# Kernel tuning notes

Hardware: AMD Instinct MI355X
Metric: run time of the kernel (lower is better)

Reference implementation:

```python
import jax, jax.numpy as jnp
import numpy as np

DECAY = 0.99
EPS = 1e-5
COMMIT_W = 1.0


def setup_inputs() -> dict:
    key = jax.random.key(0)
    k1, k2, k3 = jax.random.split(key, 3)
    N, D, K = 65536, 64, 2048
    x = jax.random.normal(k1, (N, D), dtype=jnp.float32)
    embed = jax.random.normal(k2, (K, D), dtype=jnp.float32)
    embed_avg = jax.random.normal(k3, (K, D), dtype=jnp.float32)
    cluster_size = jnp.ones((K,), dtype=jnp.float32)
    return {"x": x, "embed": embed, "embed_avg": embed_avg, "cluster_size": cluster_size}


def reference(x, embed, embed_avg, cluster_size):
    # x: [N, D], embed: [K, D]
    K = embed.shape[0]
    # squared euclidean distances [N, K] (the cdist step)
    x2 = jnp.sum(x * x, axis=-1, keepdims=True)            # [N, 1]
    e2 = jnp.sum(embed * embed, axis=-1)                    # [K]
    dist = x2 - 2.0 * (x @ embed.T) + e2[None, :]           # [N, K]
    embed_ind = jnp.argmin(dist, axis=-1)                   # [N]

    # codebook gather + straight-through estimator
    quantize = embed[embed_ind]                              # [N, D]
    commit_loss = COMMIT_W * jnp.mean((jax.lax.stop_gradient(quantize) - x) ** 2)
    quantize_st = x + jax.lax.stop_gradient(quantize - x)

    # EMA codebook update (scatter / segment-sum, no gradient)
    ones = jnp.ones(embed_ind.shape, dtype=x.dtype)
    counts = jax.ops.segment_sum(ones, embed_ind, num_segments=K)        # [K]
    embed_sum = jax.ops.segment_sum(x, embed_ind, num_segments=K)        # [K, D]
    new_cluster_size = DECAY * cluster_size + (1.0 - DECAY) * counts
    new_embed_avg = DECAY * embed_avg + (1.0 - DECAY) * embed_sum
    n = jnp.sum(new_cluster_size)
    smoothed = (new_cluster_size + EPS) / (n + K * EPS) * n              # laplace smoothing
    new_embed = new_embed_avg / smoothed[:, None]                         # [K, D]

    return quantize_st, commit_loss, embed_ind, new_embed
```

## Files before the change

### kernel.cpp

```cpp
#include <hip/hip_runtime.h>
#include <hip/hip_bf16.h>

#define N_ROWS 65536
#define DIM 64
#define KC 2048
#define NPHH 16
#define DECAY_F 0.99f
#define OMD_F 0.01f
#define EPS_F 1e-5f
#define MARGIN 0.005f

typedef short  s16x8  __attribute__((ext_vector_type(8)));
typedef __bf16 bf16x8 __attribute__((ext_vector_type(8)));
typedef float  f32x4v __attribute__((ext_vector_type(4)));

__device__ __forceinline__ bf16x8 as_bf(s16x8 v) { return __builtin_bit_cast(bf16x8, v); }

static constexpr size_t WS_E2       = 0;
static constexpr size_t WS_SMOOTH   = 2048;
static constexpr size_t WS_OFFS     = 4096;
static constexpr size_t WS_ROWIDS   = 6144;
static constexpr size_t WS_EH       = 71680;
static constexpr size_t WS_EL       = 137216;
static constexpr size_t WS_COUNTS   = 202752;
static constexpr size_t WS_CURS     = 204800;
static constexpr size_t WS_LOSS     = 206848;
static constexpr size_t WS_FLAGCNT  = 206849;
static constexpr size_t WS_ESUM     = 206852;
static constexpr size_t WS_FLAGLIST = 337924;
static constexpr size_t WS_ZERO_CNT = 4098;

__device__ __forceinline__ unsigned short bf16_rne(float f) {
    unsigned u = __float_as_uint(f);
    return (unsigned short)((u + 0x7FFFu + ((u >> 16) & 1u)) >> 16);
}

__global__ __launch_bounds__(256) void vq_prep_e_kernel(
    const float* __restrict__ embed, float* __restrict__ ws) {
    const int tid = threadIdx.x;
    const int lane = tid & 63;
    const int k = blockIdx.x * 4 + (tid >> 6);

    const int gtid = blockIdx.x * 256 + tid;
    if (gtid < (int)WS_ZERO_CNT) ws[WS_COUNTS + gtid] = 0.f;
    ws[WS_ESUM + gtid] = 0.f;

    float v = embed[(size_t)k * DIM + lane];
    float m2v = -2.f * v;
    unsigned short hb = bf16_rne(m2v);
    float hf = __uint_as_float((unsigned)hb << 16);
    unsigned short lb = bf16_rne(m2v - hf);
    ((short*)(ws + WS_EH))[(size_t)k * DIM + lane] = (short)hb;
    ((short*)(ws + WS_EL))[(size_t)k * DIM + lane] = (short)lb;

    float sq = v * v;
#pragma unroll
    for (int off = 32; off > 0; off >>= 1)
        sq += __shfl_down(sq, off, 64);
    if (lane == 0) ws[WS_E2 + k] = sq;
}

__global__ __launch_bounds__(512, 4) void vq_mfma_kernel(
    const float* __restrict__ x,
    const float* __restrict__ embed,
    float* __restrict__ ws,
    float* __restrict__ out_q,
    float* __restrict__ out_ind) {
    __shared__ __attribute__((aligned(16))) short tile_lds[2][2][16][512];
    __shared__ __attribute__((aligned(16))) float e2_lds[KC];
    __shared__ float mb1[128], mb2[128];
    __shared__ int   mi1[128];

    const int tid = threadIdx.x;
    const int lane = tid & 63;
    const int w = tid >> 6;
    const int kh = w >> 2;
    const int wq = w & 3;
    const int row0 = blockIdx.x * 128 + wq * 32;
    const int cr = lane & 15;
    const int g = lane >> 4;

    {
        const float4* s4p = reinterpret_cast<const float4*>(ws + WS_E2);
        *reinterpret_cast<float4*>(&e2_lds[tid * 4]) = s4p[tid];
    }

    s16x8 xh[2][2], xl[2][2];
#pragma unroll
    for (int f = 0; f < 2; ++f) {
#pragma unroll
        for (int kc = 0; kc < 2; ++kc) {
            const float4* p4 = reinterpret_cast<const float4*>(
                x + (size_t)(row0 + f * 16 + cr) * DIM + kc * 32 + g * 8);
            float4 u = p4[0], v = p4[1];
            s16x8 h, l;
            unsigned short hb;
            hb = bf16_rne(u.x); h[0] = (short)hb; l[0] = (short)bf16_rne(u.x - __uint_as_float((unsigned)hb << 16));
            hb = bf16_rne(u.y); h[1] = (short)hb; l[1] = (short)bf16_rne(u.y - __uint_as_float((unsigned)hb << 16));
            hb = bf16_rne(u.z); h[2] = (short)hb; l[2] = (short)bf16_rne(u.z - __uint_as_float((unsigned)hb << 16));
            hb = bf16_rne(u.w); h[3] = (short)hb; l[3] = (short)bf16_rne(u.w - __uint_as_float((unsigned)hb << 16));
            hb = bf16_rne(v.x); h[4] = (short)hb; l[4] = (short)bf16_rne(v.x - __uint_as_float((unsigned)hb << 16));
            hb = bf16_rne(v.y); h[5] = (short)hb; l[5] = (short)bf16_rne(v.y - __uint_as_float((unsigned)hb << 16));
            hb = bf16_rne(v.z); h[6] = (short)hb; l[6] = (short)bf16_rne(v.z - __uint_as_float((unsigned)hb << 16));
            hb = bf16_rne(v.w); h[7] = (short)hb; l[7] = (short)bf16_rne(v.w - __uint_as_float((unsigned)hb << 16));
            xh[f][kc] = h; xl[f][kc] = l;
        }
    }

    const short* ehp = (const short*)(ws + WS_EH);
    const short* elp = (const short*)(ws + WS_EL);

    const short* mat_base = ((wq < 2) ? ehp : elp) + (wq & 1) * 32;

#define STAGE(buf, ph)                                                                  \
    {                                                                                   \
        _Pragma("unroll")                                                               \
        for (int s4 = 0; s4 < 4; ++s4) {                                                \
            const short* gsrc = mat_base +                                              \
                (size_t)(((kh * NPHH + (ph)) * 64) + s4 * 16 + cr) * DIM + g * 8;       \
            __builtin_amdgcn_global_load_lds(                                           \
                (const __attribute__((address_space(1))) void*)gsrc,                    \
                (__attribute__((address_space(3))) void*)(&tile_lds[(buf)][kh][s4 * 4 + wq][0]), \
                16, 0, 0);                                                              \
        }                                                                               \
    }

    STAGE(0, 0);
    __syncthreads();

    float b1[2] = {__builtin_inff(), __builtin_inff()};
    float b2[2] = {__builtin_inff(), __builtin_inff()};
    int   i1[2] = {0, 0};

    for (int ph = 0; ph < NPHH; ++ph) {
        const int cur = ph & 1;
        if (ph + 1 < NPHH) STAGE(cur ^ 1, ph + 1);

        __builtin_amdgcn_s_setprio(1);
#pragma unroll
        for (int s = 0; s < 4; ++s) {
            s16x8 eh0 = *(const s16x8*)(&tile_lds[cur][kh][s * 4 + 0][lane * 8]);
            s16x8 eh1 = *(const s16x8*)(&tile_lds[cur][kh][s * 4 + 1][lane * 8]);
            s16x8 el0 = *(const s16x8*)(&tile_lds[cur][kh][s * 4 + 2][lane * 8]);
            s16x8 el1 = *(const s16x8*)(&tile_lds[cur][kh][s * 4 + 3][lane * 8]);

            const int kb = (kh * NPHH + ph) * 64 + s * 16 + g * 4;
            f32x4v e2v = *reinterpret_cast<const f32x4v*>(&e2_lds[kb]);

#pragma unroll
            for (int f = 0; f < 2; ++f) {
                f32x4v a = e2v;
                a = __builtin_amdgcn_mfma_f32_16x16x32_bf16(as_bf(eh0), as_bf(xh[f][0]), a, 0, 0, 0);
                a = __builtin_amdgcn_mfma_f32_16x16x32_bf16(as_bf(eh1), as_bf(xh[f][1]), a, 0, 0, 0);
                a = __builtin_amdgcn_mfma_f32_16x16x32_bf16(as_bf(el0), as_bf(xh[f][0]), a, 0, 0, 0);
                a = __builtin_amdgcn_mfma_f32_16x16x32_bf16(as_bf(el1), as_bf(xh[f][1]), a, 0, 0, 0);
                a = __builtin_amdgcn_mfma_f32_16x16x32_bf16(as_bf(eh0), as_bf(xl[f][0]), a, 0, 0, 0);
                a = __builtin_amdgcn_mfma_f32_16x16x32_bf16(as_bf(eh1), as_bf(xl[f][1]), a, 0, 0, 0);

#pragma unroll
                for (int r = 0; r < 4; ++r) {
                    float dd = a[r];
                    b2[f] = __builtin_amdgcn_fmed3f(b1[f], b2[f], dd);
                    if (dd < b1[f]) { b1[f] = dd; i1[f] = kb + r; }
                }
            }
        }
        __builtin_amdgcn_s_setprio(0);
        __syncthreads();
    }
#undef STAGE

#pragma unroll
    for (int f = 0; f < 2; ++f) {
#pragma unroll
        for (int mask = 16; mask <= 32; mask <<= 1) {
            float ob1 = __shfl_xor(b1[f], mask, 64);
            int   oi1 = __shfl_xor(i1[f], mask, 64);
            float ob2 = __shfl_xor(b2[f], mask, 64);
            float nb2 = fminf(fminf(b2[f], ob2), fmaxf(b1[f], ob1));
            if (ob1 < b1[f] || (ob1 == b1[f] && oi1 < i1[f])) { b1[f] = ob1; i1[f] = oi1; }
            b2[f] = nb2;
        }
    }

    if (kh == 1 && g == 0) {
#pragma unroll
        for (int f = 0; f < 2; ++f) {
            int rib = wq * 32 + f * 16 + cr;
            mb1[rib] = b1[f];
            mb2[rib] = b2[f];
            mi1[rib] = i1[f];
        }
    }
    __syncthreads();
    if (kh == 1) return;

    float gap[2];
#pragma unroll
    for (int f = 0; f < 2; ++f) {
        int rib = wq * 32 + f * 16 + cr;
        float ob1 = mb1[rib];
        float ob2 = mb2[rib];
        int   oi1 = mi1[rib];
        float nb2 = fminf(fminf(b2[f], ob2), fmaxf(b1[f], ob1));
        if (ob1 < b1[f]) { b1[f] = ob1; i1[f] = oi1; }
        b2[f] = nb2;
        gap[f] = b2[f] - b1[f];
        if (g == 0) {
            int row = row0 + f * 16 + cr;
            out_ind[row] = (float)i1[f];
            if (gap[f] < MARGIN) {
                int p = atomicAdd((int*)(ws + WS_FLAGCNT), 1);
                if (p >= 0 && p < N_ROWS) ((int*)(ws + WS_FLAGLIST))[p] = row;
            } else {
                atomicAdd((int*)(ws + WS_COUNTS) + i1[f], 1);
            }
        }
    }

    float lossacc = 0.f;
#pragma unroll
    for (int f = 0; f < 2; ++f) {
#pragma unroll
        for (int r = 0; r < 16; ++r) {
            int   fi_r = __shfl(i1[f], r, 64);
            float gp_r = __shfl(gap[f], r, 64);
            if (gp_r >= MARGIN) {
                int row = row0 + f * 16 + r;
                float q  = embed[(size_t)fi_r * DIM + lane];
                float xv = x[(size_t)row * DIM + lane];
                out_q[(size_t)row * DIM + lane] = q;
                float d = q - xv;
                lossacc = fmaf(d, d, lossacc);
            }
        }
    }
#pragma unroll
    for (int off = 32; off > 0; off >>= 1)
        lossacc += __shfl_down(lossacc, off, 64);
    if (lane == 0) atomicAdd(ws + WS_LOSS, lossacc);
}

__global__ __launch_bounds__(256) void vq_rescore_kernel(
    const float* __restrict__ x,
    const float* __restrict__ embed,
    float* __restrict__ ws,
    float* __restrict__ out_q,
    float* __restrict__ out_ind) {
    __shared__ float xs[DIM];
    __shared__ float bd[256];
    __shared__ int   bi[256];
    __shared__ int   smi;
    const int tid = threadIdx.x;
    int cnt = ((const int*)(ws + WS_FLAGCNT))[0];
    cnt = (cnt < 0) ? 0 : ((cnt > N_ROWS) ? N_ROWS : cnt);
    const int* flags = (const int*)(ws + WS_FLAGLIST);

    for (int f = blockIdx.x; f < cnt; f += gridDim.x) {
        const int row = flags[f] & (N_ROWS - 1);
        if (tid < DIM) xs[tid] = x[(size_t)row * DIM + tid];
        __syncthreads();
        float lb = __builtin_inff(); int li = 0;
        for (int k = tid; k < KC; k += 256) {
            const float* e = embed + (size_t)k * DIM;
            float dot = 0.f;
#pragma unroll
            for (int d = 0; d < DIM; ++d) dot = fmaf(xs[d], e[d], dot);
            float dd = ws[WS_E2 + k] - 2.f * dot;
            if (dd < lb) { lb = dd; li = k; }
        }
        bd[tid] = lb; bi[tid] = li;
        __syncthreads();
        for (int s = 128; s > 0; s >>= 1) {
            if (tid < s) {
                float ov = bd[tid + s]; int oi = bi[tid + s];
                if (ov < bd[tid] || (ov == bd[tid] && oi < bi[tid])) { bd[tid] = ov; bi[tid] = oi; }
            }
            __syncthreads();
        }
        if (tid == 0) {
            out_ind[row] = (float)bi[0];
            smi = bi[0];
            atomicAdd((int*)(ws + WS_COUNTS) + bi[0], 1);
        }
        __syncthreads();
        const int mi = smi;
        if (tid < DIM) {
            float q = embed[(size_t)mi * DIM + tid];
            float xv = xs[tid];
            out_q[(size_t)row * DIM + tid] = q;
            float d = q - xv;
            float ld = d * d;
#pragma unroll
            for (int off = 32; off > 0; off >>= 1)
                ld += __shfl_down(ld, off, 64);
            if (tid == 0) atomicAdd(ws + WS_LOSS, ld);
        }
        __syncthreads();
    }
}

__global__ __launch_bounds__(256) void vq_prefix_kernel(
    const float* __restrict__ cluster_size,
    float* __restrict__ ws,
    float* __restrict__ out_loss) {
    __shared__ int   sscan[256];
    __shared__ float sred[256];
    const int tid = threadIdx.x;
    const int* counts = (const int*)(ws + WS_COUNTS);
    int* offs = (int*)(ws + WS_OFFS);

    int lc[8];
    int tot = 0;
    float csum = 0.f;
#pragma unroll
    for (int j = 0; j < 8; ++j) {
        lc[j] = counts[tid * 8 + j];
        tot += lc[j];
        csum += cluster_size[tid * 8 + j];
    }
    sscan[tid] = tot;
    sred[tid] = csum;
    __syncthreads();
    for (int off = 1; off < 256; off <<= 1) {
        int v = (tid >= off) ? sscan[tid - off] : 0;
        __syncthreads();
        sscan[tid] += v;
        __syncthreads();
    }
    for (int s = 128; s > 0; s >>= 1) {
        if (tid < s) sred[tid] += sred[tid + s];
        __syncthreads();
    }
    int run = sscan[tid] - tot;
#pragma unroll
    for (int j = 0; j < 8; ++j) {
        offs[tid * 8 + j] = run;
        run += lc[j];
    }
    const float n = DECAY_F * sred[0] + OMD_F * (float)N_ROWS;
    const float scale = n / (n + (float)KC * EPS_F);
#pragma unroll
    for (int j = 0; j < 8; ++j) {
        int k = tid * 8 + j;
        float ncs = fmaf(OMD_F, (float)counts[k], DECAY_F * cluster_size[k]);
        ws[WS_SMOOTH + k] = (ncs + EPS_F) * scale;
    }
    if (tid == 0) out_loss[0] = ws[WS_LOSS] / (float)((size_t)N_ROWS * DIM);
}

__global__ __launch_bounds__(256) void vq_fill_kernel(
    const float* __restrict__ out_ind,
    float* __restrict__ ws) {
    const int row = blockIdx.x * blockDim.x + threadIdx.x;
    const int fi = ((int)out_ind[row]) & (KC - 1);
    const int* offs = (const int*)(ws + WS_OFFS);
    int* curs = (int*)(ws + WS_CURS);
    int* rowids = (int*)(ws + WS_ROWIDS);
    int pos = atomicAdd(&curs[fi], 1);
    int idx = offs[fi] + pos;
    if (idx >= 0 && idx < N_ROWS) rowids[idx] = row | (fi << 16);
}

__global__ __launch_bounds__(256) void vq_gather_kernel(
    const float* __restrict__ x,
    float* __restrict__ ws) {
    const int lane = threadIdx.x & 63;
    const int w = blockIdx.x * 4 + (threadIdx.x >> 6);
    const int* rowids = (const int*)(ws + WS_ROWIDS);
    float* esum = ws + WS_ESUM;

    const int e = rowids[w * 32 + (lane & 31)];

    float pf[8];
#pragma unroll
    for (int j = 0; j < 8; ++j) {
        int rj = __shfl(e, j, 64) & 0xFFFF;
        pf[j] = x[(size_t)rj * DIM + lane];
    }

    float acc = 0.f;
    int kprev = (__shfl(e, 0, 64) >> 16) & (KC - 1);
#pragma unroll
    for (int i = 0; i < 32; ++i) {
        float v = pf[i & 7];
        if (i + 8 < 32) {
            int rn = __shfl(e, i + 8, 64) & 0xFFFF;
            pf[i & 7] = x[(size_t)rn * DIM + lane];
        }
        int k = (__shfl(e, i, 64) >> 16) & (KC - 1);
        if (k != kprev) {
            atomicAdd(&esum[(size_t)kprev * DIM + lane], acc);
            acc = 0.f;
            kprev = k;
        }
        acc += v;
    }
    atomicAdd(&esum[(size_t)kprev * DIM + lane], acc);
}

__global__ __launch_bounds__(256) void vq_emb_kernel(
    const float* __restrict__ embed_avg,
    const float* __restrict__ ws,
    float* __restrict__ out_embed) {
    int i = blockIdx.x * blockDim.x + threadIdx.x;
    if (i >= KC * DIM) return;
    int k = i >> 6;
    float na = fmaf(OMD_F, ws[WS_ESUM + i], DECAY_F * embed_avg[i]);
    out_embed[i] = na / ws[WS_SMOOTH + k];
}

extern "C" void kernel_launch(void* const* d_in, const int* in_sizes, int n_in,
                              void* d_out, int out_size, void* d_ws, size_t ws_size,
                              hipStream_t stream) {
    const float* x            = (const float*)d_in[0];
    const float* embed        = (const float*)d_in[1];
    const float* embed_avg    = (const float*)d_in[2];
    const float* cluster_size = (const float*)d_in[3];

    float* out      = (float*)d_out;
    float* out_q    = out;
    float* out_loss = out + (size_t)N_ROWS * DIM;
    float* out_ind  = out_loss + 1;
    float* out_emb  = out_ind + N_ROWS;

    float* ws = (float*)d_ws;

    vq_prep_e_kernel<<<KC / 4, 256, 0, stream>>>(embed, ws);
    vq_mfma_kernel<<<N_ROWS / 128, 512, 0, stream>>>(x, embed, ws, out_q, out_ind);
    vq_rescore_kernel<<<2048, 256, 0, stream>>>(x, embed, ws, out_q, out_ind);
    vq_prefix_kernel<<<1, 256, 0, stream>>>(cluster_size, ws, out_loss);
    vq_fill_kernel<<<N_ROWS / 256, 256, 0, stream>>>(out_ind, ws);
    vq_gather_kernel<<<N_ROWS / 32 / 4, 256, 0, stream>>>(x, ws);
    vq_emb_kernel<<<(KC * DIM) / 256, 256, 0, stream>>>(embed_avg, ws, out_emb);
}
```

Measured before the change: 146.5 us.

## Fuse EMA embed finalization into gather via per-cluster completion counters

Removes the separate embedding-update kernel. The prefix kernel computes how many 32-row chunks touch each cluster and stores that in a remaining-count array; it also writes outputs directly for empty clusters. In the gather kernel, each flush decrements the cluster's counter after a threadfence, and the last contributor reads the accumulated sum and writes the final embedding. This saves one launch and a full pass over esum, at the cost of an extra atomic and fence per flush and serial per-thread loops in the single-block prefix kernel for empty clusters.

```diff
diff --git a/kernel.cpp b/kernel.cpp
--- a/kernel.cpp
+++ b/kernel.cpp
@@ -28,6 +28,7 @@
 static constexpr size_t WS_FLAGCNT  = 206849;
 static constexpr size_t WS_ESUM     = 206852;
 static constexpr size_t WS_FLAGLIST = 337924;
+static constexpr size_t WS_REM      = 403460;
 static constexpr size_t WS_ZERO_CNT = 4098;
 
 __device__ __forceinline__ unsigned short bf16_rne(float f) {
@@ -302,13 +303,16 @@
 
 __global__ __launch_bounds__(256) void vq_prefix_kernel(
     const float* __restrict__ cluster_size,
+    const float* __restrict__ embed_avg,
     float* __restrict__ ws,
-    float* __restrict__ out_loss) {
+    float* __restrict__ out_loss,
+    float* __restrict__ out_embed) {
     __shared__ int   sscan[256];
     __shared__ float sred[256];
     const int tid = threadIdx.x;
     const int* counts = (const int*)(ws + WS_COUNTS);
     int* offs = (int*)(ws + WS_OFFS);
+    int* rem  = (int*)(ws + WS_REM);
 
     int lc[8];
     int tot = 0;
@@ -333,18 +337,25 @@
         __syncthreads();
     }
     int run = sscan[tid] - tot;
-#pragma unroll
-    for (int j = 0; j < 8; ++j) {
-        offs[tid * 8 + j] = run;
-        run += lc[j];
-    }
     const float n = DECAY_F * sred[0] + OMD_F * (float)N_ROWS;
     const float scale = n / (n + (float)KC * EPS_F);
 #pragma unroll
     for (int j = 0; j < 8; ++j) {
         int k = tid * 8 + j;
-        float ncs = fmaf(OMD_F, (float)counts[k], DECAY_F * cluster_size[k]);
-        ws[WS_SMOOTH + k] = (ncs + EPS_F) * scale;
+        int start = run;
+        offs[k] = start;
+        run += lc[j];
+        float ncs = fmaf(OMD_F, (float)lc[j], DECAY_F * cluster_size[k]);
+        float sm = (ncs + EPS_F) * scale;
+        ws[WS_SMOOTH + k] = sm;
+        if (lc[j] > 0) {
+            rem[k] = ((start + lc[j] - 1) >> 5) - (start >> 5) + 1;
+        } else {
+            rem[k] = 0;
+            const float inv = DECAY_F / sm;
+            for (int d = 0; d < DIM; ++d)
+                out_embed[(size_t)k * DIM + d] = embed_avg[(size_t)k * DIM + d] * inv;
+        }
     }
     if (tid == 0) out_loss[0] = ws[WS_LOSS] / (float)((size_t)N_ROWS * DIM);
 }
@@ -364,11 +375,14 @@
 
 __global__ __launch_bounds__(256) void vq_gather_kernel(
     const float* __restrict__ x,
-    float* __restrict__ ws) {
+    const float* __restrict__ embed_avg,
+    float* __restrict__ ws,
+    float* __restrict__ out_embed) {
     const int lane = threadIdx.x & 63;
     const int w = blockIdx.x * 4 + (threadIdx.x >> 6);
     const int* rowids = (const int*)(ws + WS_ROWIDS);
     float* esum = ws + WS_ESUM;
+    int* rem = (int*)(ws + WS_REM);
 
     const int e = rowids[w * 32 + (lane & 31)];
 
@@ -377,6 +391,20 @@
     for (int j = 0; j < 8; ++j) {
         int rj = __shfl(e, j, 64) & 0xFFFF;
         pf[j] = x[(size_t)rj * DIM + lane];
+    }
+
+#define FLUSH(kk, accv)                                                                  \
+    {                                                                                    \
+        atomicAdd(&esum[(size_t)(kk) * DIM + lane], (accv));                             \
+        __threadfence();                                                                 \
+        int old_ = 0;                                                                    \
+        if (lane == 0) old_ = atomicSub(&rem[(kk)], 1);                                  \
+        old_ = __shfl(old_, 0, 64);                                                      \
+        if (old_ == 1) {                                                                 \
+            float val_ = esum[(size_t)(kk) * DIM + lane];                                \
+            float na_ = fmaf(OMD_F, val_, DECAY_F * embed_avg[(size_t)(kk) * DIM + lane]); \
+            out_embed[(size_t)(kk) * DIM + lane] = na_ / ws[WS_SMOOTH + (kk)];           \
+        }                                                                                \
     }
 
     float acc = 0.f;
@@ -390,24 +418,14 @@
         }
         int k = (__shfl(e, i, 64) >> 16) & (KC - 1);
         if (k != kprev) {
-            atomicAdd(&esum[(size_t)kprev * DIM + lane], acc);
+            FLUSH(kprev, acc);
             acc = 0.f;
             kprev = k;
         }
         acc += v;
     }
-    atomicAdd(&esum[(size_t)kprev * DIM + lane], acc);
-}
-
-__global__ __launch_bounds__(256) void vq_emb_kernel(
-    const float* __restrict__ embed_avg,
-    const float* __restrict__ ws,
-    float* __restrict__ out_embed) {
-    int i = blockIdx.x * blockDim.x + threadIdx.x;
-    if (i >= KC * DIM) return;
-    int k = i >> 6;
-    float na = fmaf(OMD_F, ws[WS_ESUM + i], DECAY_F * embed_avg[i]);
-    out_embed[i] = na / ws[WS_SMOOTH + k];
+    FLUSH(kprev, acc);
+#undef FLUSH
 }
 
 extern "C" void kernel_launch(void* const* d_in, const int* in_sizes, int n_in,
@@ -429,8 +447,7 @@
     vq_prep_e_kernel<<<KC / 4, 256, 0, stream>>>(embed, ws);
     vq_mfma_kernel<<<N_ROWS / 128, 512, 0, stream>>>(x, embed, ws, out_q, out_ind);
     vq_rescore_kernel<<<2048, 256, 0, stream>>>(x, embed, ws, out_q, out_ind);
-    vq_prefix_kernel<<<1, 256, 0, stream>>>(cluster_size, ws, out_loss);
+    vq_prefix_kernel<<<1, 256, 0, stream>>>(cluster_size, embed_avg, ws, out_loss, out_emb);
     vq_fill_kernel<<<N_ROWS / 256, 256, 0, stream>>>(out_ind, ws);
-    vq_gather_kernel<<<N_ROWS / 32 / 4, 256, 0, stream>>>(x, ws);
-    vq_emb_kernel<<<(KC * DIM) / 256, 256, 0, stream>>>(embed_avg, ws, out_emb);
-}
+    vq_gather_kernel<<<N_ROWS / 32 / 4, 256, 0, stream>>>(x, embed_avg, ws, out_emb);
+}
```

Result: slower. 238.4 us (+62.7%).

## Software-pipeline MFMA distance phases with argmin selection across double accumulators

Applied to the files above, without the earlier changes.

Splits each codebook phase into an MFMA stage that writes distances into one of two accumulator sets and a selection stage that scans them. The selection for phase p now runs after the MFMAs for phase p+1 are issued, so the VALU compare/fmed3 work can overlap matrix-core latency instead of waiting on each accumulator chain. This doubles the live accumulator registers (two 4x2 sets of f32x4), which may raise VGPR pressure and lower occupancy.

```diff
diff --git a/kernel.cpp b/kernel.cpp
--- a/kernel.cpp
+++ b/kernel.cpp
@@ -132,42 +132,68 @@
     float b2[2] = {__builtin_inff(), __builtin_inff()};
     int   i1[2] = {0, 0};
 
-    for (int ph = 0; ph < NPHH; ++ph) {
-        const int cur = ph & 1;
-        if (ph + 1 < NPHH) STAGE(cur ^ 1, ph + 1);
-
-        __builtin_amdgcn_s_setprio(1);
-#pragma unroll
-        for (int s = 0; s < 4; ++s) {
-            s16x8 eh0 = *(const s16x8*)(&tile_lds[cur][kh][s * 4 + 0][lane * 8]);
-            s16x8 eh1 = *(const s16x8*)(&tile_lds[cur][kh][s * 4 + 1][lane * 8]);
-            s16x8 el0 = *(const s16x8*)(&tile_lds[cur][kh][s * 4 + 2][lane * 8]);
-            s16x8 el1 = *(const s16x8*)(&tile_lds[cur][kh][s * 4 + 3][lane * 8]);
-
-            const int kb = (kh * NPHH + ph) * 64 + s * 16 + g * 4;
-            f32x4v e2v = *reinterpret_cast<const f32x4v*>(&e2_lds[kb]);
-
-#pragma unroll
-            for (int f = 0; f < 2; ++f) {
-                f32x4v a = e2v;
-                a = __builtin_amdgcn_mfma_f32_16x16x32_bf16(as_bf(eh0), as_bf(xh[f][0]), a, 0, 0, 0);
-                a = __builtin_amdgcn_mfma_f32_16x16x32_bf16(as_bf(eh1), as_bf(xh[f][1]), a, 0, 0, 0);
-                a = __builtin_amdgcn_mfma_f32_16x16x32_bf16(as_bf(el0), as_bf(xh[f][0]), a, 0, 0, 0);
-                a = __builtin_amdgcn_mfma_f32_16x16x32_bf16(as_bf(el1), as_bf(xh[f][1]), a, 0, 0, 0);
-                a = __builtin_amdgcn_mfma_f32_16x16x32_bf16(as_bf(eh0), as_bf(xl[f][0]), a, 0, 0, 0);
-                a = __builtin_amdgcn_mfma_f32_16x16x32_bf16(as_bf(eh1), as_bf(xl[f][1]), a, 0, 0, 0);
-
-#pragma unroll
-                for (int r = 0; r < 4; ++r) {
-                    float dd = a[r];
-                    b2[f] = __builtin_amdgcn_fmed3f(b1[f], b2[f], dd);
-                    if (dd < b1[f]) { b1[f] = dd; i1[f] = kb + r; }
-                }
-            }
-        }
-        __builtin_amdgcn_s_setprio(0);
-        __syncthreads();
-    }
+    f32x4v accA[4][2], accB[4][2];
+
+#define MFMA_PHASE(ph, WACC)                                                            \
+    {                                                                                   \
+        const int cur_ = (ph) & 1;                                                      \
+        if ((ph) + 1 < NPHH) STAGE(cur_ ^ 1, (ph) + 1);                                 \
+        __builtin_amdgcn_s_setprio(1);                                                  \
+        _Pragma("unroll")                                                               \
+        for (int s = 0; s < 4; ++s) {                                                   \
+            s16x8 eh0 = *(const s16x8*)(&tile_lds[cur_][kh][s * 4 + 0][lane * 8]);      \
+            s16x8 eh1 = *(const s16x8*)(&tile_lds[cur_][kh][s * 4 + 1][lane * 8]);      \
+            s16x8 el0 = *(const s16x8*)(&tile_lds[cur_][kh][s * 4 + 2][lane * 8]);      \
+            s16x8 el1 = *(const s16x8*)(&tile_lds[cur_][kh][s * 4 + 3][lane * 8]);      \
+            const int kb_ = (kh * NPHH + (ph)) * 64 + s * 16 + g * 4;                   \
+            f32x4v e2v = *reinterpret_cast<const f32x4v*>(&e2_lds[kb_]);                \
+            _Pragma("unroll")                                                           \
+            for (int f = 0; f < 2; ++f) {                                               \
+                f32x4v a = e2v;                                                         \
+                a = __builtin_amdgcn_mfma_f32_16x16x32_bf16(as_bf(eh0), as_bf(xh[f][0]), a, 0, 0, 0); \
+                a = __builtin_amdgcn_mfma_f32_16x16x32_bf16(as_bf(eh1), as_bf(xh[f][1]), a, 0, 0, 0); \
+                a = __builtin_amdgcn_mfma_f32_16x16x32_bf16(as_bf(el0), as_bf(xh[f][0]), a, 0, 0, 0); \
+                a = __builtin_amdgcn_mfma_f32_16x16x32_bf16(as_bf(el1), as_bf(xh[f][1]), a, 0, 0, 0); \
+                a = __builtin_amdgcn_mfma_f32_16x16x32_bf16(as_bf(eh0), as_bf(xl[f][0]), a, 0, 0, 0); \
+                a = __builtin_amdgcn_mfma_f32_16x16x32_bf16(as_bf(eh1), as_bf(xl[f][1]), a, 0, 0, 0); \
+                WACC[s][f] = a;                                                         \
+            }                                                                           \
+        }                                                                               \
+        __builtin_amdgcn_s_setprio(0);                                                  \
+    }
+
+#define SELECT_PHASE(ph, RACC)                                                          \
+    {                                                                                   \
+        _Pragma("unroll")                                                               \
+        for (int s = 0; s < 4; ++s) {                                                   \
+            const int kb_ = (kh * NPHH + (ph)) * 64 + s * 16 + g * 4;                   \
+            _Pragma("unroll")                                                           \
+            for (int f = 0; f < 2; ++f) {                                               \
+                _Pragma("unroll")                                                       \
+                for (int r = 0; r < 4; ++r) {                                           \
+                    float dd = RACC[s][f][r];                                           \
+                    b2[f] = __builtin_amdgcn_fmed3f(b1[f], b2[f], dd);                  \
+                    if (dd < b1[f]) { b1[f] = dd; i1[f] = kb_ + r; }                    \
+                }                                                                       \
+            }                                                                           \
+        }                                                                               \
+    }
+
+    MFMA_PHASE(0, accA);
+    __syncthreads();
+    for (int ph = 1; ph < NPHH - 1; ph += 2) {
+        MFMA_PHASE(ph, accB);
+        SELECT_PHASE(ph - 1, accA);
+        __syncthreads();
+        MFMA_PHASE(ph + 1, accA);
+        SELECT_PHASE(ph, accB);
+        __syncthreads();
+    }
+    MFMA_PHASE(NPHH - 1, accB);
+    SELECT_PHASE(NPHH - 2, accA);
+    SELECT_PHASE(NPHH - 1, accB);
+#undef MFMA_PHASE
+#undef SELECT_PHASE
 #undef STAGE
 
 #pragma unroll
```

After: 144.0 us, median of 2. No clear change (-1.7%).
